# Kernel tuning notes

Measured on AMD Instinct MI355X. Metric: run time of the kernel, lower is better.

Reference implementation:

```python
import jax, jax.numpy as jnp
import numpy as np

N_TOKENS = 2048
HIDDEN = 2048
N_EXPERTS = 8
TOP_K = 2
D_FF = 1408  # per-expert SwiGLU intermediate size


def setup_inputs() -> dict:
    key = jax.random.key(0)
    k_h, k_g, k_wg, k_wu, k_wd = jax.random.split(key, 5)
    s_in = 1.0 / np.sqrt(HIDDEN)
    s_ff = 1.0 / np.sqrt(D_FF)
    return {
        "h": jax.random.normal(k_h, (N_TOKENS, HIDDEN), dtype=jnp.float32),
        "gate_w": jax.random.normal(k_g, (N_EXPERTS, HIDDEN), dtype=jnp.float32) * s_in,
        "w_gate": jax.random.normal(k_wg, (N_EXPERTS, HIDDEN, D_FF), dtype=jnp.float32) * s_in,
        "w_up": jax.random.normal(k_wu, (N_EXPERTS, HIDDEN, D_FF), dtype=jnp.float32) * s_in,
        "w_down": jax.random.normal(k_wd, (N_EXPERTS, D_FF, HIDDEN), dtype=jnp.float32) * s_ff,
    }


def reference(h, gate_w, w_gate, w_up, w_down):
    # --- gate: linear (fp32) + softmax + top-k (no renorm, as in source) ---
    logits = jnp.einsum("nd,ed->ne", h.astype(jnp.float32), gate_w.astype(jnp.float32))
    scores = jax.nn.softmax(logits, axis=-1)                 # [N, E]
    topk_weight, topk_idx = jax.lax.top_k(scores, TOP_K)     # [N, K], [N, K]

    # --- per-expert SwiGLU MLP applied densely, then gather selected experts ---
    # (same math as the per-expert grouped GEMM dispatch in the eager loop)
    g = jnp.einsum("nd,edf->enf", h, w_gate)                 # [E, N, F]
    u = jnp.einsum("nd,edf->enf", h, w_up)                   # [E, N, F]
    y = jnp.einsum("enf,efd->end", jax.nn.silu(g) * u, w_down)  # [E, N, D]

    # gather each token's top-k expert outputs: [N, K, D]
    y_tok = jnp.transpose(y, (1, 0, 2))                      # [N, E, D]
    sel = jnp.take_along_axis(y_tok, topk_idx[:, :, None], axis=1)

    # weighted combine
    out = jnp.einsum("nk,nkd->nd", topk_weight.astype(h.dtype), sel)
    return out
```

## Files before the change

kernel.cpp:

```cpp
#include <hip/hip_runtime.h>
#include <hip/hip_bf16.h>
#include <stdint.h>

#define N_TOK 2048
#define HID   2048
#define NEXP  8
#define DFF   1408

typedef __attribute__((ext_vector_type(8))) short short8;
typedef __attribute__((ext_vector_type(4))) float f32x4;

__device__ __forceinline__ unsigned short f2bf(float f) {
  union { float ff; uint32_t u; } v; v.ff = f;
  return (unsigned short)((v.u + 0x7FFFu + ((v.u >> 16) & 1u)) >> 16);
}

__device__ __forceinline__ void gl2lds16(const void* g, void* l) {
  __builtin_amdgcn_global_load_lds(
      (const __attribute__((address_space(1))) void*)g,
      (__attribute__((address_space(3))) void*)l, 16, 0, 0);
}

__global__ __launch_bounds__(256) void gate_topk_k(
    const float* __restrict__ h, const float* __restrict__ gw,
    int* __restrict__ cnt, int* __restrict__ topk_idx, float* __restrict__ topk_w)
{
  int token = blockIdx.x * 4 + (threadIdx.x >> 6);
  int lane  = threadIdx.x & 63;
  const float* hr = h + (size_t)token * HID;
  float acc[NEXP];
#pragma unroll
  for (int e = 0; e < NEXP; ++e) acc[e] = 0.f;
  for (int i = lane; i < HID; i += 64) {
    float hv = hr[i];
#pragma unroll
    for (int e = 0; e < NEXP; ++e) acc[e] = fmaf(hv, gw[e * HID + i], acc[e]);
  }
#pragma unroll
  for (int e = 0; e < NEXP; ++e) {
    float a = acc[e];
#pragma unroll
    for (int s = 32; s > 0; s >>= 1) a += __shfl_xor(a, s, 64);
    acc[e] = a;
  }
  if (lane == 0) {
    float m = acc[0];
#pragma unroll
    for (int e = 1; e < NEXP; ++e) m = fmaxf(m, acc[e]);
    float w[NEXP]; float s = 0.f;
#pragma unroll
    for (int e = 0; e < NEXP; ++e) { w[e] = __expf(acc[e] - m); s += w[e]; }
    float inv = 1.f / s;
    int i0 = 0; float b0 = acc[0];
#pragma unroll
    for (int e = 1; e < NEXP; ++e) if (acc[e] > b0) { b0 = acc[e]; i0 = e; }
    int i1 = -1; float b1 = -3.4e38f;
#pragma unroll
    for (int e = 0; e < NEXP; ++e) if (e != i0 && acc[e] > b1) { b1 = acc[e]; i1 = e; }
    topk_idx[token * 2 + 0] = i0;
    topk_idx[token * 2 + 1] = i1;
    topk_w[token * 2 + 0] = w[i0] * inv;
    topk_w[token * 2 + 1] = w[i1] * inv;
    atomicAdd(&cnt[i0], 1);
    atomicAdd(&cnt[i1], 1);
  }
}

__global__ void prefix_k(const int* __restrict__ cnt, int* __restrict__ offs,
                         int* __restrict__ cursor) {
  if (threadIdx.x == 0 && blockIdx.x == 0) {
    int s = 0;
    for (int e = 0; e < NEXP; ++e) { offs[e] = s; cursor[e] = s; s += cnt[e]; }
  }
}

__global__ __launch_bounds__(256) void scatter_k(
    const int* __restrict__ topk_idx, const float* __restrict__ topk_w,
    int* __restrict__ cursor, int* __restrict__ pair_token, float* __restrict__ pair_w,
    int* __restrict__ tok_slot)
{
  int n = blockIdx.x * 256 + threadIdx.x;
  if (n >= N_TOK) return;
#pragma unroll
  for (int k = 0; k < 2; ++k) {
    int e = topk_idx[n * 2 + k];
    int p = atomicAdd(&cursor[e], 1);
    pair_token[p] = n;
    pair_w[p] = topk_w[n * 2 + k];
    tok_slot[n * 2 + k] = p;
  }
}

__global__ __launch_bounds__(256) void convert_h_k(const float* __restrict__ src,
                                                   unsigned short* __restrict__ dst) {
  int i = blockIdx.x * 256 + threadIdx.x;
  float4 a = ((const float4*)src)[(size_t)i * 2];
  float4 b = ((const float4*)src)[(size_t)i * 2 + 1];
  unsigned short o[8] = {f2bf(a.x), f2bf(a.y), f2bf(a.z), f2bf(a.w),
                         f2bf(b.x), f2bf(b.y), f2bf(b.z), f2bf(b.w)};
  *(short8*)&dst[(size_t)i * 8] = *(const short8*)o;
}

__global__ __launch_bounds__(256) void transpose_k(const float* __restrict__ s1,
                                                   unsigned short* __restrict__ d1,
                                                   const float* __restrict__ s2,
                                                   unsigned short* __restrict__ d2,
                                                   int R, int C, int nz1)
{
  __shared__ unsigned short T[64 * 66];
  const size_t sl = (size_t)R * C;
  int z = blockIdx.z;
  const float* s; unsigned short* d;
  if (z < nz1) { s = s1 + (size_t)z * sl; d = d1 + (size_t)z * sl; }
  else { s = s2 + (size_t)(z - nz1) * sl; d = d2 + (size_t)(z - nz1) * sl; }
  const int rb = blockIdx.x * 64, cb = blockIdx.y * 64;
  const int t = threadIdx.x;
  const int tr = t >> 4, tc = (t & 15) * 4;
  const float* sp = s + (size_t)(rb + tr) * C + cb + tc;
#pragma unroll
  for (int i = 0; i < 4; ++i) {
    float4 v = *(const float4*)(sp + (size_t)i * 16 * C);
    int r = tr + i * 16;
    uint32_t p0 = (uint32_t)f2bf(v.x) | ((uint32_t)f2bf(v.y) << 16);
    uint32_t p1 = (uint32_t)f2bf(v.z) | ((uint32_t)f2bf(v.w) << 16);
    *(uint32_t*)&T[r * 66 + tc]     = p0;
    *(uint32_t*)&T[r * 66 + tc + 2] = p1;
  }
  __syncthreads();
  const int f = t >> 2, ch = (t & 3) * 16;
  unsigned short* dp = d + (size_t)(cb + f) * R + rb + ch;
#pragma unroll
  for (int g = 0; g < 2; ++g) {
    unsigned short buf[8];
#pragma unroll
    for (int j = 0; j < 8; ++j) buf[j] = T[(ch + g * 8 + j) * 66 + f];
    *(short8*)(dp + g * 8) = *(const short8*)buf;
  }
}

__global__ __launch_bounds__(512) void gateup5_k(
    const unsigned short* __restrict__ hbf,
    const unsigned short* __restrict__ wgt, const unsigned short* __restrict__ wut,
    const int* __restrict__ cnt, const int* __restrict__ offs,
    const int* __restrict__ pair_token, unsigned short* __restrict__ act,
    int e_fixed, int nw, int nbcnt, size_t wstride)
{
  const int x = blockIdx.x;
  const int wti = x % nw, mb = x / nw;
  int e, nb;
  if (e_fixed >= 0) { e = e_fixed; nb = wti; }
  else { e = wti / nbcnt; nb = wti % nbcnt; }
  const int count = cnt[e];
  if (mb * 128 >= count) return;
  const int off = offs[e];
  const int rows = min(128, count - mb * 128);
  const int c0 = nb * 128;

  __shared__ unsigned short As[2][128 * 64];
  __shared__ unsigned short Bg[2][128 * 64];
  __shared__ unsigned short Bu[2][128 * 64];
  __shared__ int tok[128];

  const int t = threadIdx.x;
  if (t < 128) tok[t] = pair_token[off + mb * 128 + min(t, rows - 1)];
  __syncthreads();

  const int w = t >> 6, l = t & 63;
  const int sr = l >> 3;
  const int sc = ((l & 7) ^ sr) * 8;
  const int r0 = w * 16 + sr, r1 = w * 16 + 8 + sr;

  const size_t wb = (e_fixed >= 0) ? 0 : (size_t)e * wstride;
  const unsigned short* wgE = wgt + wb;
  const unsigned short* wuE = wut + wb;
  const unsigned short* aP0 = hbf + (size_t)tok[r0] * HID + sc;
  const unsigned short* aP1 = hbf + (size_t)tok[r1] * HID + sc;
  const unsigned short* gP0 = wgE + (size_t)(c0 + r0) * HID + sc;
  const unsigned short* gP1 = wgE + (size_t)(c0 + r1) * HID + sc;
  const unsigned short* uP0 = wuE + (size_t)(c0 + r0) * HID + sc;
  const unsigned short* uP1 = wuE + (size_t)(c0 + r1) * HID + sc;
  const int ldsLo = (w * 16) * 64, ldsHi = (w * 16 + 8) * 64;

  const int fr = l & 15, fq = l >> 4;
  const int wr = (w >> 2) * 64, wc = (w & 3) * 32;
  const int f3 = fr & 7;

  f32x4 accg[4][2], accu[4][2];
#pragma unroll
  for (int i = 0; i < 4; ++i)
#pragma unroll
    for (int j = 0; j < 2; ++j) {
      accg[i][j] = (f32x4){0.f, 0.f, 0.f, 0.f};
      accu[i][j] = (f32x4){0.f, 0.f, 0.f, 0.f};
    }

  auto stage = [&](int b, int kt) {
    gl2lds16(aP0 + kt, &As[b][ldsLo]); gl2lds16(aP1 + kt, &As[b][ldsHi]);
    gl2lds16(gP0 + kt, &Bg[b][ldsLo]); gl2lds16(gP1 + kt, &Bg[b][ldsHi]);
    gl2lds16(uP0 + kt, &Bu[b][ldsLo]); gl2lds16(uP1 + kt, &Bu[b][ldsHi]);
  };
  auto compute = [&](int b) {
    short8 af[4][2], bg[2][2], bu[2][2];
#pragma unroll
    for (int kk = 0; kk < 2; ++kk) {
      const int ch = ((kk * 4 + fq) ^ f3) * 8;
#pragma unroll
      for (int mi = 0; mi < 4; ++mi)
        af[mi][kk] = *(const short8*)&As[b][(wr + mi * 16 + fr) * 64 + ch];
#pragma unroll
      for (int ni = 0; ni < 2; ++ni) {
        bg[ni][kk] = *(const short8*)&Bg[b][(wc + ni * 16 + fr) * 64 + ch];
        bu[ni][kk] = *(const short8*)&Bu[b][(wc + ni * 16 + fr) * 64 + ch];
      }
    }
    __builtin_amdgcn_s_setprio(1);
#pragma unroll
    for (int kk = 0; kk < 2; ++kk)
#pragma unroll
      for (int mi = 0; mi < 4; ++mi)
#pragma unroll
        for (int ni = 0; ni < 2; ++ni) {
          accg[mi][ni] = __builtin_amdgcn_mfma_f32_16x16x32_bf16(af[mi][kk], bg[ni][kk], accg[mi][ni], 0, 0, 0);
          accu[mi][ni] = __builtin_amdgcn_mfma_f32_16x16x32_bf16(af[mi][kk], bu[ni][kk], accu[mi][ni], 0, 0, 0);
        }
    __builtin_amdgcn_s_setprio(0);
  };

  const int NK = HID / 64;
  stage(0, 0);
  int cur = 0;
  for (int k = 0; k + 1 < NK; ++k) {
    stage(cur ^ 1, (k + 1) * 64);
    asm volatile("s_waitcnt vmcnt(6)" ::: "memory");
    asm volatile("s_barrier" ::: "memory");
    compute(cur);
    asm volatile("s_barrier" ::: "memory");
    cur ^= 1;
  }
  asm volatile("s_waitcnt vmcnt(0)" ::: "memory");
  asm volatile("s_barrier" ::: "memory");
  compute(cur);

#pragma unroll
  for (int mi = 0; mi < 4; ++mi)
#pragma unroll
    for (int ni = 0; ni < 2; ++ni)
#pragma unroll
      for (int j = 0; j < 4; ++j) {
        int r = wr + mi * 16 + fq * 4 + j;
        if (r < rows) {
          float g = accg[mi][ni][j], u = accu[mi][ni][j];
          float a = (g / (1.f + __expf(-g))) * u;
          act[(size_t)(off + mb * 128 + r) * DFF + (c0 + wc + ni * 16 + fr)] = f2bf(a);
        }
      }
}

__global__ __launch_bounds__(256) void down5_k(
    const unsigned short* __restrict__ act, const unsigned short* __restrict__ wdt,
    const int* __restrict__ cnt, const int* __restrict__ offs,
    float* __restrict__ ypair, int e_fixed, int nw, int nbcnt, size_t wstride)
{
  const int x = blockIdx.x;
  const int wti = x % nw, mb = x / nw;
  int e, nb;
  if (e_fixed >= 0) { e = e_fixed; nb = wti; }
  else { e = wti / nbcnt; nb = wti % nbcnt; }
  const int count = cnt[e];
  if (mb * 128 >= count) return;
  const int off = offs[e];
  const int rows = min(128, count - mb * 128);
  const int c0 = nb * 128;

  __shared__ unsigned short As[2][128 * 64];
  __shared__ unsigned short Bd[2][128 * 64];

  const int t = threadIdx.x;
  const int w = t >> 6, l = t & 63;
  const int sr = l >> 3;
  const int sc = ((l & 7) ^ sr) * 8;
  const size_t wb = (e_fixed >= 0) ? 0 : (size_t)e * wstride;
  const unsigned short* wdE = wdt + wb;

  const unsigned short* aP[4];
  const unsigned short* bP[4];
  int ldsB[4];
#pragma unroll
  for (int i = 0; i < 4; ++i) {
    int rr = w * 32 + i * 8 + sr;
    aP[i] = act + (size_t)(off + mb * 128 + rr) * DFF + sc;
    bP[i] = wdE + (size_t)(c0 + rr) * DFF + sc;
    ldsB[i] = (w * 32 + i * 8) * 64;
  }

  const int fr = l & 15, fq = l >> 4;
  const int wr = (w >> 1) * 64, wc = (w & 1) * 64;
  const int f3 = fr & 7;

  f32x4 acc[4][4];
#pragma unroll
  for (int i = 0; i < 4; ++i)
#pragma unroll
    for (int j = 0; j < 4; ++j) acc[i][j] = (f32x4){0.f, 0.f, 0.f, 0.f};

  auto stage = [&](int b, int kt) {
#pragma unroll
    for (int i = 0; i < 4; ++i) {
      gl2lds16(aP[i] + kt, &As[b][ldsB[i]]);
      gl2lds16(bP[i] + kt, &Bd[b][ldsB[i]]);
    }
  };
  auto compute = [&](int b) {
    short8 af[4][2], bd[4][2];
#pragma unroll
    for (int kk = 0; kk < 2; ++kk) {
      const int ch = ((kk * 4 + fq) ^ f3) * 8;
#pragma unroll
      for (int mi = 0; mi < 4; ++mi)
        af[mi][kk] = *(const short8*)&As[b][(wr + mi * 16 + fr) * 64 + ch];
#pragma unroll
      for (int ni = 0; ni < 4; ++ni)
        bd[ni][kk] = *(const short8*)&Bd[b][(wc + ni * 16 + fr) * 64 + ch];
    }
    __builtin_amdgcn_s_setprio(1);
#pragma unroll
    for (int kk = 0; kk < 2; ++kk)
#pragma unroll
      for (int mi = 0; mi < 4; ++mi)
#pragma unroll
        for (int ni = 0; ni < 4; ++ni)
          acc[mi][ni] = __builtin_amdgcn_mfma_f32_16x16x32_bf16(af[mi][kk], bd[ni][kk], acc[mi][ni], 0, 0, 0);
    __builtin_amdgcn_s_setprio(0);
  };

  const int NK = DFF / 64;
  stage(0, 0);
  int cur = 0;
  for (int k = 0; k + 1 < NK; ++k) {
    stage(cur ^ 1, (k + 1) * 64);
    asm volatile("s_waitcnt vmcnt(8)" ::: "memory");
    asm volatile("s_barrier" ::: "memory");
    compute(cur);
    asm volatile("s_barrier" ::: "memory");
    cur ^= 1;
  }
  asm volatile("s_waitcnt vmcnt(0)" ::: "memory");
  asm volatile("s_barrier" ::: "memory");
  compute(cur);

#pragma unroll
  for (int mi = 0; mi < 4; ++mi)
#pragma unroll
    for (int ni = 0; ni < 4; ++ni)
#pragma unroll
      for (int j = 0; j < 4; ++j) {
        int r = wr + mi * 16 + fq * 4 + j;
        if (r < rows)
          ypair[(size_t)(off + mb * 128 + r) * HID + (c0 + wc + ni * 16 + fr)] = acc[mi][ni][j];
      }
}

__global__ __launch_bounds__(256) void combine_k(
    const float* __restrict__ ypair, const int* __restrict__ tok_slot,
    const float* __restrict__ topk_w, float* __restrict__ out)
{
  int i = blockIdx.x * 256 + threadIdx.x;
  int n = i >> 9;
  int dv = (i & 511) * 4;
  int s0 = tok_slot[n * 2], s1 = tok_slot[n * 2 + 1];
  float w0 = topk_w[n * 2], w1 = topk_w[n * 2 + 1];
  float4 a = *(const float4*)&ypair[(size_t)s0 * HID + dv];
  float4 b = *(const float4*)&ypair[(size_t)s1 * HID + dv];
  float4 o;
  o.x = w0 * a.x + w1 * b.x; o.y = w0 * a.y + w1 * b.y;
  o.z = w0 * a.z + w1 * b.z; o.w = w0 * a.w + w1 * b.w;
  *(float4*)&out[(size_t)n * HID + dv] = o;
}

extern "C" void kernel_launch(void* const* d_in, const int* in_sizes, int n_in,
                              void* d_out, int out_size, void* d_ws, size_t ws_size,
                              hipStream_t stream) {
  const float* h  = (const float*)d_in[0];
  const float* gw = (const float*)d_in[1];
  const float* wg = (const float*)d_in[2];
  const float* wu = (const float*)d_in[3];
  const float* wd = (const float*)d_in[4];
  float* out = (float*)d_out;

  const size_t SL = (size_t)DFF * HID;
  char* ws = (char*)d_ws;
  int*   cnt        = (int*)(ws + 0);
  int*   offs       = (int*)(ws + 32);
  int*   cursor     = (int*)(ws + 64);
  int*   pair_token = (int*)(ws + 256);
  float* pair_w     = (float*)(ws + 16640);
  int*   tok_slot   = (int*)(ws + 33024);
  int*   topk_idx   = (int*)(ws + 49408);
  float* topk_w     = (float*)(ws + 65792);
  unsigned short* act = (unsigned short*)(ws + 82176);
  unsigned short* hbf = (unsigned short*)(ws + 11616512);
  unsigned short* wgt = (unsigned short*)(ws + 20005120);
  unsigned short* wut = (unsigned short*)(ws + 66142464);
  float* ypair_full   = (float*)(ws + 66142464);
  const size_t NEED_FULL = 112279808ull;

  hipMemsetAsync(ws, 0, 256, stream);

  gate_topk_k<<<N_TOK / 4, 256, 0, stream>>>(h, gw, cnt, topk_idx, topk_w);
  prefix_k<<<1, 64, 0, stream>>>(cnt, offs, cursor);
  scatter_k<<<N_TOK / 256, 256, 0, stream>>>(topk_idx, topk_w, cursor, pair_token, pair_w, tok_slot);
  convert_h_k<<<(N_TOK * HID / 8) / 256, 256, 0, stream>>>(h, hbf);

  if (ws_size >= NEED_FULL) {
    transpose_k<<<dim3(HID / 64, DFF / 64, 16), 256, 0, stream>>>(wg, wgt, wu, wut, HID, DFF, 8);
    gateup5_k<<<88 * 16, 512, 0, stream>>>(hbf, wgt, wut, cnt, offs, pair_token, act,
                                           -1, 88, 11, SL);
    transpose_k<<<dim3(DFF / 64, HID / 64, 8), 256, 0, stream>>>(wd, wgt, wd, wgt, DFF, HID, 8);
    down5_k<<<128 * 16, 256, 0, stream>>>(act, wgt, cnt, offs, ypair_full,
                                          -1, 128, 16, SL);
    combine_k<<<(N_TOK * HID / 4) / 256, 256, 0, stream>>>(ypair_full, tok_slot, topk_w, out);
  } else {
    unsigned short* wgtE = (unsigned short*)(ws + 20005120);
    unsigned short* wutE = (unsigned short*)(ws + 25772288);
    float* ypair = (float*)(ws + 31539456);
    for (int e = 0; e < NEXP; ++e) {
      transpose_k<<<dim3(HID / 64, DFF / 64, 2), 256, 0, stream>>>(wg + e * SL, wgtE, wu + e * SL, wutE, HID, DFF, 1);
      gateup5_k<<<11 * 16, 512, 0, stream>>>(hbf, wgtE, wutE, cnt, offs, pair_token, act,
                                             e, 11, 11, 0);
    }
    for (int e = 0; e < NEXP; ++e) {
      transpose_k<<<dim3(DFF / 64, HID / 64, 1), 256, 0, stream>>>(wd + e * SL, wgtE, wd + e * SL, wgtE, DFF, HID, 1);
      down5_k<<<16 * 16, 256, 0, stream>>>(act, wgtE, cnt, offs, ypair, e, 16, 16, 0);
    }
    combine_k<<<(N_TOK * HID / 4) / 256, 256, 0, stream>>>(ypair, tok_slot, topk_w, out);
  }
}
```

Before: 322.4 us.

## Pre-pack expert weights into MFMA fragment layout and load B directly to registers

The weight preprocessing kernel now emits bf16 weights already arranged in per-lane MFMA fragment order, so the gate/up and down GEMMs read B operands straight from global memory into registers instead of staging them through LDS. Tiles shrink to 128x64 with 256-thread blocks, doubling the grid, and the main loop is unrolled by two with register double-buffering of B fragments. This removes LDS traffic and LDS footprint for B and raises occupancy. In exchange it loses B reuse across waves within a block, which adds global/L2 traffic, and it puts more pressure on registers.

```diff
diff --git a/kernel.cpp b/kernel.cpp
--- a/kernel.cpp
+++ b/kernel.cpp
@@ -101,11 +101,11 @@
   *(short8*)&dst[(size_t)i * 8] = *(const short8*)o;
 }
 
-__global__ __launch_bounds__(256) void transpose_k(const float* __restrict__ s1,
-                                                   unsigned short* __restrict__ d1,
-                                                   const float* __restrict__ s2,
-                                                   unsigned short* __restrict__ d2,
-                                                   int R, int C, int nz1)
+__global__ __launch_bounds__(256) void fragpack_k(const float* __restrict__ s1,
+                                                  unsigned short* __restrict__ d1,
+                                                  const float* __restrict__ s2,
+                                                  unsigned short* __restrict__ d2,
+                                                  int R, int C, int nz1)
 {
   __shared__ unsigned short T[64 * 66];
   const size_t sl = (size_t)R * C;
@@ -127,20 +127,25 @@
     *(uint32_t*)&T[r * 66 + tc + 2] = p1;
   }
   __syncthreads();
-  const int f = t >> 2, ch = (t & 3) * 16;
-  unsigned short* dp = d + (size_t)(cb + f) * R + rb + ch;
-#pragma unroll
-  for (int g = 0; g < 2; ++g) {
+  const int KB = R >> 5;
+#pragma unroll
+  for (int sI = 0; sI < 2; ++sI) {
+    int idx = t + sI * 256;
+    int l2 = idx & 63, kbl = (idx >> 6) & 1, fbl = idx >> 7;
+    int fr2 = l2 & 15, fq2 = l2 >> 4;
     unsigned short buf[8];
 #pragma unroll
-    for (int j = 0; j < 8; ++j) buf[j] = T[(ch + g * 8 + j) * 66 + f];
-    *(short8*)(dp + g * 8) = *(const short8*)buf;
-  }
-}
-
-__global__ __launch_bounds__(512) void gateup5_k(
+    for (int j = 0; j < 8; ++j)
+      buf[j] = T[(kbl * 32 + fq2 * 8 + j) * 66 + fbl * 16 + fr2];
+    int fbG = blockIdx.y * 4 + fbl;
+    int kbG = blockIdx.x * 2 + kbl;
+    *(short8*)(d + ((size_t)(fbG * KB + kbG) * 512 + l2 * 8)) = *(const short8*)buf;
+  }
+}
+
+__global__ __launch_bounds__(256) void gateup6_k(
     const unsigned short* __restrict__ hbf,
-    const unsigned short* __restrict__ wgt, const unsigned short* __restrict__ wut,
+    const unsigned short* __restrict__ wgp, const unsigned short* __restrict__ wup,
     const int* __restrict__ cnt, const int* __restrict__ offs,
     const int* __restrict__ pair_token, unsigned short* __restrict__ act,
     int e_fixed, int nw, int nbcnt, size_t wstride)
@@ -154,11 +159,9 @@
   if (mb * 128 >= count) return;
   const int off = offs[e];
   const int rows = min(128, count - mb * 128);
-  const int c0 = nb * 128;
+  const int c0 = nb * 64;
 
   __shared__ unsigned short As[2][128 * 64];
-  __shared__ unsigned short Bg[2][128 * 64];
-  __shared__ unsigned short Bu[2][128 * 64];
   __shared__ int tok[128];
 
   const int t = threadIdx.x;
@@ -166,24 +169,25 @@
   __syncthreads();
 
   const int w = t >> 6, l = t & 63;
-  const int sr = l >> 3;
-  const int sc = ((l & 7) ^ sr) * 8;
-  const int r0 = w * 16 + sr, r1 = w * 16 + 8 + sr;
+  const int rbase = w * 8 + (l >> 3);
+  const int sc = ((l & 7) ^ (l >> 3)) * 8;
+
+  const unsigned short* aP[4];
+#pragma unroll
+  for (int i = 0; i < 4; ++i)
+    aP[i] = hbf + (size_t)tok[i * 32 + rbase] * HID + sc;
 
   const size_t wb = (e_fixed >= 0) ? 0 : (size_t)e * wstride;
-  const unsigned short* wgE = wgt + wb;
-  const unsigned short* wuE = wut + wb;
-  const unsigned short* aP0 = hbf + (size_t)tok[r0] * HID + sc;
-  const unsigned short* aP1 = hbf + (size_t)tok[r1] * HID + sc;
-  const unsigned short* gP0 = wgE + (size_t)(c0 + r0) * HID + sc;
-  const unsigned short* gP1 = wgE + (size_t)(c0 + r1) * HID + sc;
-  const unsigned short* uP0 = wuE + (size_t)(c0 + r0) * HID + sc;
-  const unsigned short* uP1 = wuE + (size_t)(c0 + r1) * HID + sc;
-  const int ldsLo = (w * 16) * 64, ldsHi = (w * 16 + 8) * 64;
-
   const int fr = l & 15, fq = l >> 4;
-  const int wr = (w >> 2) * 64, wc = (w & 3) * 32;
-  const int f3 = fr & 7;
+  const int wr = (w >> 1) * 64, wc = (w & 1) * 32;
+  const unsigned short* bgB[2];
+  const unsigned short* buB[2];
+#pragma unroll
+  for (int ni = 0; ni < 2; ++ni) {
+    int fb = (c0 + wc) / 16 + ni;
+    bgB[ni] = wgp + wb + (size_t)fb * (HID / 32) * 512 + l * 8;
+    buB[ni] = wup + wb + (size_t)fb * (HID / 32) * 512 + l * 8;
+  }
 
   f32x4 accg[4][2], accu[4][2];
 #pragma unroll
@@ -194,24 +198,28 @@
       accu[i][j] = (f32x4){0.f, 0.f, 0.f, 0.f};
     }
 
-  auto stage = [&](int b, int kt) {
-    gl2lds16(aP0 + kt, &As[b][ldsLo]); gl2lds16(aP1 + kt, &As[b][ldsHi]);
-    gl2lds16(gP0 + kt, &Bg[b][ldsLo]); gl2lds16(gP1 + kt, &Bg[b][ldsHi]);
-    gl2lds16(uP0 + kt, &Bu[b][ldsLo]); gl2lds16(uP1 + kt, &Bu[b][ldsHi]);
-  };
-  auto compute = [&](int b) {
-    short8 af[4][2], bg[2][2], bu[2][2];
+  auto stage = [&](int b, int k) {
+#pragma unroll
+    for (int i = 0; i < 4; ++i)
+      gl2lds16(aP[i] + k * 64, &As[b][(i * 32 + w * 8) * 64]);
+  };
+  auto loadB = [&](short8 (&bg)[2][2], short8 (&bu)[2][2], int k) {
+#pragma unroll
+    for (int kk = 0; kk < 2; ++kk)
+#pragma unroll
+      for (int ni = 0; ni < 2; ++ni) {
+        bg[ni][kk] = *(const short8*)(bgB[ni] + (size_t)(k * 2 + kk) * 512);
+        bu[ni][kk] = *(const short8*)(buB[ni] + (size_t)(k * 2 + kk) * 512);
+      }
+  };
+  auto compute = [&](int b, short8 (&bg)[2][2], short8 (&bu)[2][2]) {
+    short8 af[4][2];
 #pragma unroll
     for (int kk = 0; kk < 2; ++kk) {
-      const int ch = ((kk * 4 + fq) ^ f3) * 8;
+      const int ch = ((kk * 4 + fq) ^ (fr & 7)) * 8;
 #pragma unroll
       for (int mi = 0; mi < 4; ++mi)
         af[mi][kk] = *(const short8*)&As[b][(wr + mi * 16 + fr) * 64 + ch];
-#pragma unroll
-      for (int ni = 0; ni < 2; ++ni) {
-        bg[ni][kk] = *(const short8*)&Bg[b][(wc + ni * 16 + fr) * 64 + ch];
-        bu[ni][kk] = *(const short8*)&Bu[b][(wc + ni * 16 + fr) * 64 + ch];
-      }
     }
     __builtin_amdgcn_s_setprio(1);
 #pragma unroll
@@ -226,20 +234,29 @@
     __builtin_amdgcn_s_setprio(0);
   };
 
+  short8 g0[2][2], u0[2][2], g1[2][2], u1[2][2];
   const int NK = HID / 64;
-  stage(0, 0);
-  int cur = 0;
-  for (int k = 0; k + 1 < NK; ++k) {
-    stage(cur ^ 1, (k + 1) * 64);
-    asm volatile("s_waitcnt vmcnt(6)" ::: "memory");
-    asm volatile("s_barrier" ::: "memory");
-    compute(cur);
-    asm volatile("s_barrier" ::: "memory");
-    cur ^= 1;
-  }
+  stage(0, 0); loadB(g0, u0, 0);
+  for (int k = 0; k + 2 < NK; k += 2) {
+    stage(1, k + 1); loadB(g1, u1, k + 1);
+    asm volatile("s_waitcnt vmcnt(12)" ::: "memory");
+    asm volatile("s_barrier" ::: "memory");
+    compute(0, g0, u0);
+    asm volatile("s_barrier" ::: "memory");
+    stage(0, k + 2); loadB(g0, u0, k + 2);
+    asm volatile("s_waitcnt vmcnt(12)" ::: "memory");
+    asm volatile("s_barrier" ::: "memory");
+    compute(1, g1, u1);
+    asm volatile("s_barrier" ::: "memory");
+  }
+  stage(1, NK - 1); loadB(g1, u1, NK - 1);
+  asm volatile("s_waitcnt vmcnt(12)" ::: "memory");
+  asm volatile("s_barrier" ::: "memory");
+  compute(0, g0, u0);
+  asm volatile("s_barrier" ::: "memory");
   asm volatile("s_waitcnt vmcnt(0)" ::: "memory");
   asm volatile("s_barrier" ::: "memory");
-  compute(cur);
+  compute(1, g1, u1);
 
 #pragma unroll
   for (int mi = 0; mi < 4; ++mi)
@@ -256,8 +273,8 @@
       }
 }
 
-__global__ __launch_bounds__(256) void down5_k(
-    const unsigned short* __restrict__ act, const unsigned short* __restrict__ wdt,
+__global__ __launch_bounds__(256) void down6_k(
+    const unsigned short* __restrict__ act, const unsigned short* __restrict__ wdp,
     const int* __restrict__ cnt, const int* __restrict__ offs,
     float* __restrict__ ypair, int e_fixed, int nw, int nbcnt, size_t wstride)
 {
@@ -270,57 +287,56 @@
   if (mb * 128 >= count) return;
   const int off = offs[e];
   const int rows = min(128, count - mb * 128);
-  const int c0 = nb * 128;
+  const int c0 = nb * 64;
 
   __shared__ unsigned short As[2][128 * 64];
-  __shared__ unsigned short Bd[2][128 * 64];
 
   const int t = threadIdx.x;
   const int w = t >> 6, l = t & 63;
-  const int sr = l >> 3;
-  const int sc = ((l & 7) ^ sr) * 8;
+  const int rbase = w * 8 + (l >> 3);
+  const int sc = ((l & 7) ^ (l >> 3)) * 8;
+
+  const unsigned short* aP[4];
+#pragma unroll
+  for (int i = 0; i < 4; ++i)
+    aP[i] = act + (size_t)(off + mb * 128 + i * 32 + rbase) * DFF + sc;
+
   const size_t wb = (e_fixed >= 0) ? 0 : (size_t)e * wstride;
-  const unsigned short* wdE = wdt + wb;
-
-  const unsigned short* aP[4];
-  const unsigned short* bP[4];
-  int ldsB[4];
-#pragma unroll
-  for (int i = 0; i < 4; ++i) {
-    int rr = w * 32 + i * 8 + sr;
-    aP[i] = act + (size_t)(off + mb * 128 + rr) * DFF + sc;
-    bP[i] = wdE + (size_t)(c0 + rr) * DFF + sc;
-    ldsB[i] = (w * 32 + i * 8) * 64;
-  }
-
   const int fr = l & 15, fq = l >> 4;
-  const int wr = (w >> 1) * 64, wc = (w & 1) * 64;
-  const int f3 = fr & 7;
-
-  f32x4 acc[4][4];
+  const int wr = (w >> 1) * 64, wc = (w & 1) * 32;
+  const unsigned short* bdB[2];
+#pragma unroll
+  for (int ni = 0; ni < 2; ++ni) {
+    int fb = (c0 + wc) / 16 + ni;
+    bdB[ni] = wdp + wb + (size_t)fb * (DFF / 32) * 512 + l * 8;
+  }
+
+  f32x4 acc[4][2];
 #pragma unroll
   for (int i = 0; i < 4; ++i)
 #pragma unroll
-    for (int j = 0; j < 4; ++j) acc[i][j] = (f32x4){0.f, 0.f, 0.f, 0.f};
-
-  auto stage = [&](int b, int kt) {
-#pragma unroll
-    for (int i = 0; i < 4; ++i) {
-      gl2lds16(aP[i] + kt, &As[b][ldsB[i]]);
-      gl2lds16(bP[i] + kt, &Bd[b][ldsB[i]]);
-    }
-  };
-  auto compute = [&](int b) {
-    short8 af[4][2], bd[4][2];
+    for (int j = 0; j < 2; ++j) acc[i][j] = (f32x4){0.f, 0.f, 0.f, 0.f};
+
+  auto stage = [&](int b, int k) {
+#pragma unroll
+    for (int i = 0; i < 4; ++i)
+      gl2lds16(aP[i] + k * 64, &As[b][(i * 32 + w * 8) * 64]);
+  };
+  auto loadB = [&](short8 (&bd)[2][2], int k) {
+#pragma unroll
+    for (int kk = 0; kk < 2; ++kk)
+#pragma unroll
+      for (int ni = 0; ni < 2; ++ni)
+        bd[ni][kk] = *(const short8*)(bdB[ni] + (size_t)(k * 2 + kk) * 512);
+  };
+  auto compute = [&](int b, short8 (&bd)[2][2]) {
+    short8 af[4][2];
 #pragma unroll
     for (int kk = 0; kk < 2; ++kk) {
-      const int ch = ((kk * 4 + fq) ^ f3) * 8;
+      const int ch = ((kk * 4 + fq) ^ (fr & 7)) * 8;
 #pragma unroll
       for (int mi = 0; mi < 4; ++mi)
         af[mi][kk] = *(const short8*)&As[b][(wr + mi * 16 + fr) * 64 + ch];
-#pragma unroll
-      for (int ni = 0; ni < 4; ++ni)
-        bd[ni][kk] = *(const short8*)&Bd[b][(wc + ni * 16 + fr) * 64 + ch];
     }
     __builtin_amdgcn_s_setprio(1);
 #pragma unroll
@@ -328,30 +344,39 @@
 #pragma unroll
       for (int mi = 0; mi < 4; ++mi)
 #pragma unroll
-        for (int ni = 0; ni < 4; ++ni)
+        for (int ni = 0; ni < 2; ++ni)
           acc[mi][ni] = __builtin_amdgcn_mfma_f32_16x16x32_bf16(af[mi][kk], bd[ni][kk], acc[mi][ni], 0, 0, 0);
     __builtin_amdgcn_s_setprio(0);
   };
 
+  short8 d0[2][2], d1[2][2];
   const int NK = DFF / 64;
-  stage(0, 0);
-  int cur = 0;
-  for (int k = 0; k + 1 < NK; ++k) {
-    stage(cur ^ 1, (k + 1) * 64);
+  stage(0, 0); loadB(d0, 0);
+  for (int k = 0; k + 2 < NK; k += 2) {
+    stage(1, k + 1); loadB(d1, k + 1);
     asm volatile("s_waitcnt vmcnt(8)" ::: "memory");
     asm volatile("s_barrier" ::: "memory");
-    compute(cur);
-    asm volatile("s_barrier" ::: "memory");
-    cur ^= 1;
-  }
+    compute(0, d0);
+    asm volatile("s_barrier" ::: "memory");
+    stage(0, k + 2); loadB(d0, k + 2);
+    asm volatile("s_waitcnt vmcnt(8)" ::: "memory");
+    asm volatile("s_barrier" ::: "memory");
+    compute(1, d1);
+    asm volatile("s_barrier" ::: "memory");
+  }
+  stage(1, NK - 1); loadB(d1, NK - 1);
+  asm volatile("s_waitcnt vmcnt(8)" ::: "memory");
+  asm volatile("s_barrier" ::: "memory");
+  compute(0, d0);
+  asm volatile("s_barrier" ::: "memory");
   asm volatile("s_waitcnt vmcnt(0)" ::: "memory");
   asm volatile("s_barrier" ::: "memory");
-  compute(cur);
+  compute(1, d1);
 
 #pragma unroll
   for (int mi = 0; mi < 4; ++mi)
 #pragma unroll
-    for (int ni = 0; ni < 4; ++ni)
+    for (int ni = 0; ni < 2; ++ni)
 #pragma unroll
       for (int j = 0; j < 4; ++j) {
         int r = wr + mi * 16 + fq * 4 + j;
@@ -412,25 +437,25 @@
   convert_h_k<<<(N_TOK * HID / 8) / 256, 256, 0, stream>>>(h, hbf);
 
   if (ws_size >= NEED_FULL) {
-    transpose_k<<<dim3(HID / 64, DFF / 64, 16), 256, 0, stream>>>(wg, wgt, wu, wut, HID, DFF, 8);
-    gateup5_k<<<88 * 16, 512, 0, stream>>>(hbf, wgt, wut, cnt, offs, pair_token, act,
-                                           -1, 88, 11, SL);
-    transpose_k<<<dim3(DFF / 64, HID / 64, 8), 256, 0, stream>>>(wd, wgt, wd, wgt, DFF, HID, 8);
-    down5_k<<<128 * 16, 256, 0, stream>>>(act, wgt, cnt, offs, ypair_full,
-                                          -1, 128, 16, SL);
+    fragpack_k<<<dim3(HID / 64, DFF / 64, 16), 256, 0, stream>>>(wg, wgt, wu, wut, HID, DFF, 8);
+    gateup6_k<<<176 * 16, 256, 0, stream>>>(hbf, wgt, wut, cnt, offs, pair_token, act,
+                                            -1, 176, 22, SL);
+    fragpack_k<<<dim3(DFF / 64, HID / 64, 8), 256, 0, stream>>>(wd, wgt, wd, wgt, DFF, HID, 8);
+    down6_k<<<256 * 16, 256, 0, stream>>>(act, wgt, cnt, offs, ypair_full,
+                                          -1, 256, 32, SL);
     combine_k<<<(N_TOK * HID / 4) / 256, 256, 0, stream>>>(ypair_full, tok_slot, topk_w, out);
   } else {
     unsigned short* wgtE = (unsigned short*)(ws + 20005120);
     unsigned short* wutE = (unsigned short*)(ws + 25772288);
     float* ypair = (float*)(ws + 31539456);
     for (int e = 0; e < NEXP; ++e) {
-      transpose_k<<<dim3(HID / 64, DFF / 64, 2), 256, 0, stream>>>(wg + e * SL, wgtE, wu + e * SL, wutE, HID, DFF, 1);
-      gateup5_k<<<11 * 16, 512, 0, stream>>>(hbf, wgtE, wutE, cnt, offs, pair_token, act,
-                                             e, 11, 11, 0);
+      fragpack_k<<<dim3(HID / 64, DFF / 64, 2), 256, 0, stream>>>(wg + e * SL, wgtE, wu + e * SL, wutE, HID, DFF, 1);
+      gateup6_k<<<22 * 16, 256, 0, stream>>>(hbf, wgtE, wutE, cnt, offs, pair_token, act,
+                                             e, 22, 22, 0);
     }
     for (int e = 0; e < NEXP; ++e) {
-      transpose_k<<<dim3(DFF / 64, HID / 64, 1), 256, 0, stream>>>(wd + e * SL, wgtE, wd + e * SL, wgtE, DFF, HID, 1);
-      down5_k<<<16 * 16, 256, 0, stream>>>(act, wgtE, cnt, offs, ypair, e, 16, 16, 0);
+      fragpack_k<<<dim3(DFF / 64, HID / 64, 1), 256, 0, stream>>>(wd + e * SL, wgtE, wd + e * SL, wgtE, DFF, HID, 1);
+      down6_k<<<32 * 16, 256, 0, stream>>>(act, wgtE, cnt, offs, ypair, e, 32, 32, 0);
     }
     combine_k<<<(N_TOK * HID / 4) / 256, 256, 0, stream>>>(ypair, tok_slot, topk_w, out);
   }
```

New measurement: 353.8 us. +9.7%, slower.

## Triple-buffer gate/up GEMM and interleave LDS reads with MFMA phases

Applied to the files above, without the earlier changes.

The gate/up expert GEMM moves from double to triple LDS buffering with a two-tile prefetch distance, and drops the trailing per-iteration barrier. Both grouped GEMMs now split each k-tile's compute into four phases that interleave smaller LDS fragment loads with MFMA bursts, separated by s_barrier and sched_barrier. The aim is to hide global-load latency and overlap LDS reads with matrix math. The cost is 50% more shared memory in the gate/up kernel, which may lower occupancy, and extra barriers per tile.

```diff
diff --git a/kernel.cpp b/kernel.cpp
--- a/kernel.cpp
+++ b/kernel.cpp
@@ -20,6 +20,8 @@
       (const __attribute__((address_space(1))) void*)g,
       (__attribute__((address_space(3))) void*)l, 16, 0, 0);
 }
+
+#define MFMA16(a, b, c) __builtin_amdgcn_mfma_f32_16x16x32_bf16((a), (b), (c), 0, 0, 0)
 
 __global__ __launch_bounds__(256) void gate_topk_k(
     const float* __restrict__ h, const float* __restrict__ gw,
@@ -138,7 +140,7 @@
   }
 }
 
-__global__ __launch_bounds__(512) void gateup5_k(
+__global__ __launch_bounds__(512) void gateup7_k(
     const unsigned short* __restrict__ hbf,
     const unsigned short* __restrict__ wgt, const unsigned short* __restrict__ wut,
     const int* __restrict__ cnt, const int* __restrict__ offs,
@@ -156,9 +158,9 @@
   const int rows = min(128, count - mb * 128);
   const int c0 = nb * 128;
 
-  __shared__ unsigned short As[2][128 * 64];
-  __shared__ unsigned short Bg[2][128 * 64];
-  __shared__ unsigned short Bu[2][128 * 64];
+  __shared__ unsigned short As[3][128 * 64];
+  __shared__ unsigned short Bg[3][128 * 64];
+  __shared__ unsigned short Bu[3][128 * 64];
   __shared__ int tok[128];
 
   const int t = threadIdx.x;
@@ -184,6 +186,8 @@
   const int fr = l & 15, fq = l >> 4;
   const int wr = (w >> 2) * 64, wc = (w & 3) * 32;
   const int f3 = fr & 7;
+  const int ch0 = (fq ^ f3) * 8;
+  const int ch1 = ((4 + fq) ^ f3) * 8;
 
   f32x4 accg[4][2], accu[4][2];
 #pragma unroll
@@ -199,47 +203,79 @@
     gl2lds16(gP0 + kt, &Bg[b][ldsLo]); gl2lds16(gP1 + kt, &Bg[b][ldsHi]);
     gl2lds16(uP0 + kt, &Bu[b][ldsLo]); gl2lds16(uP1 + kt, &Bu[b][ldsHi]);
   };
-  auto compute = [&](int b) {
-    short8 af[4][2], bg[2][2], bu[2][2];
-#pragma unroll
-    for (int kk = 0; kk < 2; ++kk) {
-      const int ch = ((kk * 4 + fq) ^ f3) * 8;
-#pragma unroll
-      for (int mi = 0; mi < 4; ++mi)
-        af[mi][kk] = *(const short8*)&As[b][(wr + mi * 16 + fr) * 64 + ch];
-#pragma unroll
-      for (int ni = 0; ni < 2; ++ni) {
-        bg[ni][kk] = *(const short8*)&Bg[b][(wc + ni * 16 + fr) * 64 + ch];
-        bu[ni][kk] = *(const short8*)&Bu[b][(wc + ni * 16 + fr) * 64 + ch];
-      }
+
+  auto compute4 = [&](int b) {
+    const unsigned short* as = As[b];
+    const unsigned short* gs = Bg[b];
+    const unsigned short* us = Bu[b];
+    short8 a0, a1, g0, g1, u0, u1;
+    a0 = *(const short8*)&as[(wr + fr) * 64 + ch0];
+    a1 = *(const short8*)&as[(wr + 16 + fr) * 64 + ch0];
+    g0 = *(const short8*)&gs[(wc + fr) * 64 + ch0];
+    g1 = *(const short8*)&gs[(wc + 16 + fr) * 64 + ch0];
+    u0 = *(const short8*)&us[(wc + fr) * 64 + ch0];
+    u1 = *(const short8*)&us[(wc + 16 + fr) * 64 + ch0];
+    __builtin_amdgcn_s_barrier();
+    __builtin_amdgcn_s_setprio(1);
+    accg[0][0] = MFMA16(a0, g0, accg[0][0]); accu[0][0] = MFMA16(a0, u0, accu[0][0]);
+    accg[0][1] = MFMA16(a0, g1, accg[0][1]); accu[0][1] = MFMA16(a0, u1, accu[0][1]);
+    accg[1][0] = MFMA16(a1, g0, accg[1][0]); accu[1][0] = MFMA16(a1, u0, accu[1][0]);
+    accg[1][1] = MFMA16(a1, g1, accg[1][1]); accu[1][1] = MFMA16(a1, u1, accu[1][1]);
+    __builtin_amdgcn_s_setprio(0);
+    __builtin_amdgcn_sched_barrier(0);
+    a0 = *(const short8*)&as[(wr + 32 + fr) * 64 + ch0];
+    a1 = *(const short8*)&as[(wr + 48 + fr) * 64 + ch0];
+    __builtin_amdgcn_s_barrier();
+    __builtin_amdgcn_s_setprio(1);
+    accg[2][0] = MFMA16(a0, g0, accg[2][0]); accu[2][0] = MFMA16(a0, u0, accu[2][0]);
+    accg[2][1] = MFMA16(a0, g1, accg[2][1]); accu[2][1] = MFMA16(a0, u1, accu[2][1]);
+    accg[3][0] = MFMA16(a1, g0, accg[3][0]); accu[3][0] = MFMA16(a1, u0, accu[3][0]);
+    accg[3][1] = MFMA16(a1, g1, accg[3][1]); accu[3][1] = MFMA16(a1, u1, accu[3][1]);
+    __builtin_amdgcn_s_setprio(0);
+    __builtin_amdgcn_sched_barrier(0);
+    a0 = *(const short8*)&as[(wr + fr) * 64 + ch1];
+    a1 = *(const short8*)&as[(wr + 16 + fr) * 64 + ch1];
+    g0 = *(const short8*)&gs[(wc + fr) * 64 + ch1];
+    g1 = *(const short8*)&gs[(wc + 16 + fr) * 64 + ch1];
+    u0 = *(const short8*)&us[(wc + fr) * 64 + ch1];
+    u1 = *(const short8*)&us[(wc + 16 + fr) * 64 + ch1];
+    __builtin_amdgcn_s_barrier();
+    __builtin_amdgcn_s_setprio(1);
+    accg[0][0] = MFMA16(a0, g0, accg[0][0]); accu[0][0] = MFMA16(a0, u0, accu[0][0]);
+    accg[0][1] = MFMA16(a0, g1, accg[0][1]); accu[0][1] = MFMA16(a0, u1, accu[0][1]);
+    accg[1][0] = MFMA16(a1, g0, accg[1][0]); accu[1][0] = MFMA16(a1, u0, accu[1][0]);
+    accg[1][1] = MFMA16(a1, g1, accg[1][1]); accu[1][1] = MFMA16(a1, u1, accu[1][1]);
+    __builtin_amdgcn_s_setprio(0);
+    __builtin_amdgcn_sched_barrier(0);
+    a0 = *(const short8*)&as[(wr + 32 + fr) * 64 + ch1];
+    a1 = *(const short8*)&as[(wr + 48 + fr) * 64 + ch1];
+    __builtin_amdgcn_s_barrier();
+    __builtin_amdgcn_s_setprio(1);
+    accg[2][0] = MFMA16(a0, g0, accg[2][0]); accu[2][0] = MFMA16(a0, u0, accu[2][0]);
+    accg[2][1] = MFMA16(a0, g1, accg[2][1]); accu[2][1] = MFMA16(a0, u1, accu[2][1]);
+    accg[3][0] = MFMA16(a1, g0, accg[3][0]); accu[3][0] = MFMA16(a1, u0, accu[3][0]);
+    accg[3][1] = MFMA16(a1, g1, accg[3][1]); accu[3][1] = MFMA16(a1, u1, accu[3][1]);
+    __builtin_amdgcn_s_setprio(0);
+    __builtin_amdgcn_sched_barrier(0);
+  };
+
+  const int NK = HID / 64;
+  stage(0, 0); stage(1, 64);
+  int bc = 0;
+  for (int k = 0; k < NK; ++k) {
+    if (k + 2 < NK) {
+      int bn = bc + 2; if (bn >= 3) bn -= 3;
+      stage(bn, (k + 2) * 64);
+      asm volatile("s_waitcnt vmcnt(12)" ::: "memory");
+    } else if (k + 1 < NK) {
+      asm volatile("s_waitcnt vmcnt(6)" ::: "memory");
+    } else {
+      asm volatile("s_waitcnt vmcnt(0)" ::: "memory");
     }
-    __builtin_amdgcn_s_setprio(1);
-#pragma unroll
-    for (int kk = 0; kk < 2; ++kk)
-#pragma unroll
-      for (int mi = 0; mi < 4; ++mi)
-#pragma unroll
-        for (int ni = 0; ni < 2; ++ni) {
-          accg[mi][ni] = __builtin_amdgcn_mfma_f32_16x16x32_bf16(af[mi][kk], bg[ni][kk], accg[mi][ni], 0, 0, 0);
-          accu[mi][ni] = __builtin_amdgcn_mfma_f32_16x16x32_bf16(af[mi][kk], bu[ni][kk], accu[mi][ni], 0, 0, 0);
-        }
-    __builtin_amdgcn_s_setprio(0);
-  };
-
-  const int NK = HID / 64;
-  stage(0, 0);
-  int cur = 0;
-  for (int k = 0; k + 1 < NK; ++k) {
-    stage(cur ^ 1, (k + 1) * 64);
-    asm volatile("s_waitcnt vmcnt(6)" ::: "memory");
-    asm volatile("s_barrier" ::: "memory");
-    compute(cur);
-    asm volatile("s_barrier" ::: "memory");
-    cur ^= 1;
-  }
-  asm volatile("s_waitcnt vmcnt(0)" ::: "memory");
-  asm volatile("s_barrier" ::: "memory");
-  compute(cur);
+    __builtin_amdgcn_s_barrier();
+    compute4(bc);
+    bc = (bc == 2) ? 0 : bc + 1;
+  }
 
 #pragma unroll
   for (int mi = 0; mi < 4; ++mi)
@@ -256,7 +292,7 @@
       }
 }
 
-__global__ __launch_bounds__(256) void down5_k(
+__global__ __launch_bounds__(256) void down7_k(
     const unsigned short* __restrict__ act, const unsigned short* __restrict__ wdt,
     const int* __restrict__ cnt, const int* __restrict__ offs,
     float* __restrict__ ypair, int e_fixed, int nw, int nbcnt, size_t wstride)
@@ -296,6 +332,8 @@
   const int fr = l & 15, fq = l >> 4;
   const int wr = (w >> 1) * 64, wc = (w & 1) * 64;
   const int f3 = fr & 7;
+  const int ch0 = (fq ^ f3) * 8;
+  const int ch1 = ((4 + fq) ^ f3) * 8;
 
   f32x4 acc[4][4];
 #pragma unroll
@@ -310,43 +348,76 @@
       gl2lds16(bP[i] + kt, &Bd[b][ldsB[i]]);
     }
   };
-  auto compute = [&](int b) {
-    short8 af[4][2], bd[4][2];
-#pragma unroll
-    for (int kk = 0; kk < 2; ++kk) {
-      const int ch = ((kk * 4 + fq) ^ f3) * 8;
-#pragma unroll
-      for (int mi = 0; mi < 4; ++mi)
-        af[mi][kk] = *(const short8*)&As[b][(wr + mi * 16 + fr) * 64 + ch];
-#pragma unroll
-      for (int ni = 0; ni < 4; ++ni)
-        bd[ni][kk] = *(const short8*)&Bd[b][(wc + ni * 16 + fr) * 64 + ch];
-    }
-    __builtin_amdgcn_s_setprio(1);
-#pragma unroll
-    for (int kk = 0; kk < 2; ++kk)
-#pragma unroll
-      for (int mi = 0; mi < 4; ++mi)
-#pragma unroll
-        for (int ni = 0; ni < 4; ++ni)
-          acc[mi][ni] = __builtin_amdgcn_mfma_f32_16x16x32_bf16(af[mi][kk], bd[ni][kk], acc[mi][ni], 0, 0, 0);
-    __builtin_amdgcn_s_setprio(0);
+
+  auto compute4 = [&](int b) {
+    const unsigned short* as = As[b];
+    const unsigned short* ds = Bd[b];
+    short8 a0, a1, d0, d1, d2, d3;
+    a0 = *(const short8*)&as[(wr + fr) * 64 + ch0];
+    a1 = *(const short8*)&as[(wr + 16 + fr) * 64 + ch0];
+    d0 = *(const short8*)&ds[(wc + fr) * 64 + ch0];
+    d1 = *(const short8*)&ds[(wc + 16 + fr) * 64 + ch0];
+    d2 = *(const short8*)&ds[(wc + 32 + fr) * 64 + ch0];
+    d3 = *(const short8*)&ds[(wc + 48 + fr) * 64 + ch0];
+    __builtin_amdgcn_s_barrier();
+    __builtin_amdgcn_s_setprio(1);
+    acc[0][0] = MFMA16(a0, d0, acc[0][0]); acc[0][1] = MFMA16(a0, d1, acc[0][1]);
+    acc[0][2] = MFMA16(a0, d2, acc[0][2]); acc[0][3] = MFMA16(a0, d3, acc[0][3]);
+    acc[1][0] = MFMA16(a1, d0, acc[1][0]); acc[1][1] = MFMA16(a1, d1, acc[1][1]);
+    acc[1][2] = MFMA16(a1, d2, acc[1][2]); acc[1][3] = MFMA16(a1, d3, acc[1][3]);
+    __builtin_amdgcn_s_setprio(0);
+    __builtin_amdgcn_sched_barrier(0);
+    a0 = *(const short8*)&as[(wr + 32 + fr) * 64 + ch0];
+    a1 = *(const short8*)&as[(wr + 48 + fr) * 64 + ch0];
+    __builtin_amdgcn_s_barrier();
+    __builtin_amdgcn_s_setprio(1);
+    acc[2][0] = MFMA16(a0, d0, acc[2][0]); acc[2][1] = MFMA16(a0, d1, acc[2][1]);
+    acc[2][2] = MFMA16(a0, d2, acc[2][2]); acc[2][3] = MFMA16(a0, d3, acc[2][3]);
+    acc[3][0] = MFMA16(a1, d0, acc[3][0]); acc[3][1] = MFMA16(a1, d1, acc[3][1]);
+    acc[3][2] = MFMA16(a1, d2, acc[3][2]); acc[3][3] = MFMA16(a1, d3, acc[3][3]);
+    __builtin_amdgcn_s_setprio(0);
+    __builtin_amdgcn_sched_barrier(0);
+    a0 = *(const short8*)&as[(wr + fr) * 64 + ch1];
+    a1 = *(const short8*)&as[(wr + 16 + fr) * 64 + ch1];
+    d0 = *(const short8*)&ds[(wc + fr) * 64 + ch1];
+    d1 = *(const short8*)&ds[(wc + 16 + fr) * 64 + ch1];
+    d2 = *(const short8*)&ds[(wc + 32 + fr) * 64 + ch1];
+    d3 = *(const short8*)&ds[(wc + 48 + fr) * 64 + ch1];
+    __builtin_amdgcn_s_barrier();
+    __builtin_amdgcn_s_setprio(1);
+    acc[0][0] = MFMA16(a0, d0, acc[0][0]); acc[0][1] = MFMA16(a0, d1, acc[0][1]);
+    acc[0][2] = MFMA16(a0, d2, acc[0][2]); acc[0][3] = MFMA16(a0, d3, acc[0][3]);
+    acc[1][0] = MFMA16(a1, d0, acc[1][0]); acc[1][1] = MFMA16(a1, d1, acc[1][1]);
+    acc[1][2] = MFMA16(a1, d2, acc[1][2]); acc[1][3] = MFMA16(a1, d3, acc[1][3]);
+    __builtin_amdgcn_s_setprio(0);
+    __builtin_amdgcn_sched_barrier(0);
+    a0 = *(const short8*)&as[(wr + 32 + fr) * 64 + ch1];
+    a1 = *(const short8*)&as[(wr + 48 + fr) * 64 + ch1];
+    __builtin_amdgcn_s_barrier();
+    __builtin_amdgcn_s_setprio(1);
+    acc[2][0] = MFMA16(a0, d0, acc[2][0]); acc[2][1] = MFMA16(a0, d1, acc[2][1]);
+    acc[2][2] = MFMA16(a0, d2, acc[2][2]); acc[2][3] = MFMA16(a0, d3, acc[2][3]);
+    acc[3][0] = MFMA16(a1, d0, acc[3][0]); acc[3][1] = MFMA16(a1, d1, acc[3][1]);
+    acc[3][2] = MFMA16(a1, d2, acc[3][2]); acc[3][3] = MFMA16(a1, d3, acc[3][3]);
+    __builtin_amdgcn_s_setprio(0);
+    __builtin_amdgcn_sched_barrier(0);
   };
 
   const int NK = DFF / 64;
   stage(0, 0);
   int cur = 0;
-  for (int k = 0; k + 1 < NK; ++k) {
-    stage(cur ^ 1, (k + 1) * 64);
-    asm volatile("s_waitcnt vmcnt(8)" ::: "memory");
-    asm volatile("s_barrier" ::: "memory");
-    compute(cur);
-    asm volatile("s_barrier" ::: "memory");
+  for (int k = 0; k < NK; ++k) {
+    if (k + 1 < NK) {
+      stage(cur ^ 1, (k + 1) * 64);
+      asm volatile("s_waitcnt vmcnt(8)" ::: "memory");
+    } else {
+      asm volatile("s_waitcnt vmcnt(0)" ::: "memory");
+    }
+    __builtin_amdgcn_s_barrier();
+    compute4(cur);
+    __builtin_amdgcn_s_barrier();
     cur ^= 1;
   }
-  asm volatile("s_waitcnt vmcnt(0)" ::: "memory");
-  asm volatile("s_barrier" ::: "memory");
-  compute(cur);
 
 #pragma unroll
   for (int mi = 0; mi < 4; ++mi)
@@ -413,10 +484,10 @@
 
   if (ws_size >= NEED_FULL) {
     transpose_k<<<dim3(HID / 64, DFF / 64, 16), 256, 0, stream>>>(wg, wgt, wu, wut, HID, DFF, 8);
-    gateup5_k<<<88 * 16, 512, 0, stream>>>(hbf, wgt, wut, cnt, offs, pair_token, act,
+    gateup7_k<<<88 * 16, 512, 0, stream>>>(hbf, wgt, wut, cnt, offs, pair_token, act,
                                            -1, 88, 11, SL);
     transpose_k<<<dim3(DFF / 64, HID / 64, 8), 256, 0, stream>>>(wd, wgt, wd, wgt, DFF, HID, 8);
-    down5_k<<<128 * 16, 256, 0, stream>>>(act, wgt, cnt, offs, ypair_full,
+    down7_k<<<128 * 16, 256, 0, stream>>>(act, wgt, cnt, offs, ypair_full,
                                           -1, 128, 16, SL);
     combine_k<<<(N_TOK * HID / 4) / 256, 256, 0, stream>>>(ypair_full, tok_slot, topk_w, out);
   } else {
@@ -425,12 +496,12 @@
     float* ypair = (float*)(ws + 31539456);
     for (int e = 0; e < NEXP; ++e) {
       transpose_k<<<dim3(HID / 64, DFF / 64, 2), 256, 0, stream>>>(wg + e * SL, wgtE, wu + e * SL, wutE, HID, DFF, 1);
-      gateup5_k<<<11 * 16, 512, 0, stream>>>(hbf, wgtE, wutE, cnt, offs, pair_token, act,
+      gateup7_k<<<11 * 16, 512, 0, stream>>>(hbf, wgtE, wutE, cnt, offs, pair_token, act,
                                              e, 11, 11, 0);
     }
     for (int e = 0; e < NEXP; ++e) {
       transpose_k<<<dim3(DFF / 64, HID / 64, 1), 256, 0, stream>>>(wd + e * SL, wgtE, wd + e * SL, wgtE, DFF, HID, 1);
-      down5_k<<<16 * 16, 256, 0, stream>>>(act, wgtE, cnt, offs, ypair, e, 16, 16, 0);
+      down7_k<<<16 * 16, 256, 0, stream>>>(act, wgtE, cnt, offs, ypair, e, 16, 16, 0);
     }
     combine_k<<<(N_TOK * HID / 4) / 256, 256, 0, stream>>>(ypair, tok_slot, topk_w, out);
   }
```

After: 330.4 us. 2.5% more time.
